# Kernel tuning notes

Measured on AMD Instinct MI355X. Metric: run time of the kernel, lower is better.

Reference implementation:

```python
import jax, jax.numpy as jnp
import numpy as np


def setup_inputs() -> dict:
    key = jax.random.key(0)
    k1, k2 = jax.random.split(key)
    inputs = jax.random.normal(k1, (16, 64, 64, 64), dtype=jnp.float32)  # NCHW, C=embedding_dim
    codebook = jax.random.normal(k2, (1024, 64), dtype=jnp.float32)      # [K, D]
    return {"inputs": inputs, "codebook": codebook}


def reference(inputs, codebook):
    # inputs: [B, C, H, W] -> [B, H, W, C] -> [N, D]
    D = codebook.shape[1]
    x = jnp.transpose(inputs, (0, 2, 3, 1)).reshape(-1, D)  # [N, D]
    distances = (
        jnp.sum(x * x, axis=1, keepdims=True)
        + jnp.sum(codebook * codebook, axis=1)
        - 2.0 * jnp.matmul(x, codebook.T)
    )
    encoding_indices = jnp.argmin(distances, axis=1)[:, None]  # [N, 1]
    return encoding_indices
```

## Files before the change

kernel.cpp:

```cpp
#include <hip/hip_runtime.h>


typedef float f4 __attribute__((ext_vector_type(4)));
typedef float f32x16 __attribute__((ext_vector_type(16)));
typedef short s8v __attribute__((ext_vector_type(8)));
typedef unsigned int u32;

#define D_DIM 64
#define HW    4096
#define ROWSB 128
#define INF_  __builtin_inff()
#define M32(a,b,c) __builtin_amdgcn_mfma_f32_32x32x16_bf16(a,b,c,0,0,0)
#define Z16 (f32x16){0.f,0.f,0.f,0.f,0.f,0.f,0.f,0.f,0.f,0.f,0.f,0.f,0.f,0.f,0.f,0.f}

__device__ __forceinline__ unsigned short bf_rne(float f) {
    u32 u = __builtin_bit_cast(u32, f);
    u32 r = u + 0x7fffu + ((u >> 16) & 1u);
    return (unsigned short)(r >> 16);
}
__device__ __forceinline__ float bf_to_f(unsigned short h) {
    u32 u = ((u32)h) << 16;
    return __builtin_bit_cast(float, u);
}
__device__ __forceinline__ void split3(float f, unsigned short& h,
                                       unsigned short& m, unsigned short& l) {
    h = bf_rne(f);
    float f1 = f - bf_to_f(h);
    m = bf_rne(f1);
    float f2 = f1 - bf_to_f(m);
    l = bf_rne(f2);
}
__device__ __forceinline__ s8v pack8(unsigned short a0, unsigned short a1,
                                     unsigned short a2, unsigned short a3,
                                     unsigned short a4, unsigned short a5,
                                     unsigned short a6, unsigned short a7) {
    uint4 u;
    u.x = a0 | ((u32)a1 << 16);
    u.y = a2 | ((u32)a3 << 16);
    u.z = a4 | ((u32)a5 << 16);
    u.w = a6 | ((u32)a7 << 16);
    return __builtin_bit_cast(s8v, u);
}

__global__ __launch_bounds__(64) void prep_kernel(const float* __restrict__ cb,
                                                  char* __restrict__ wsb) {
    const int blk = blockIdx.x;
    const int lane = threadIdx.x;
    if (blk < 384) {
        const int T = blk / 12;
        const int rem = blk - T * 12;
        const int s = rem / 3;
        const int L = rem - s * 3;
        const int code = T * 32 + (lane & 31);
        const int ch0 = s * 16 + (lane >> 5) * 8;
        const float* src = cb + code * 64 + ch0;
        unsigned short o[8];
#pragma unroll
        for (int j = 0; j < 8; ++j) {
            unsigned short h, m2, l;
            split3(src[j], h, m2, l);
            o[j] = (L == 0) ? h : (L == 1) ? m2 : l;
        }
        uint4 w;
        w.x = o[0] | ((u32)o[1] << 16);
        w.y = o[2] | ((u32)o[3] << 16);
        w.z = o[4] | ((u32)o[5] << 16);
        w.w = o[6] | ((u32)o[7] << 16);
        *(uint4*)(wsb + (size_t)blk * 1024 + lane * 16) = w;
    } else {
        const int k = (blk - 384) * 64 + lane;
        const f4* row = (const f4*)(cb + (size_t)k * 64);
        float sacc = 0.f;
#pragma unroll
        for (int i = 0; i < 16; ++i) {
            f4 v = row[i];
            sacc = fmaf(v.x, v.x, sacc);
            sacc = fmaf(v.y, v.y, sacc);
            sacc = fmaf(v.z, v.z, sacc);
            sacc = fmaf(v.w, v.w, sacc);
        }
        ((float*)(wsb + 384 * 1024))[k] = sacc;
    }
}

__device__ __forceinline__ void gl_lds16(const char* g, char* l) {
    __builtin_amdgcn_global_load_lds(
        (const __attribute__((address_space(1))) void*)g,
        (__attribute__((address_space(3))) void*)l, 16, 0, 0);
}

#define BUILD_A(s) { \
    const float* xr = (const float*)&xs4[w32 + l31][0]; \
    f4 va = *(const f4*)(xr + (s) * 16 + lh8); \
    f4 vb = *(const f4*)(xr + (s) * 16 + lh8 + 4); \
    unsigned short h0,h1,h2,h3,h4,h5,h6,h7; \
    unsigned short q0,q1,q2,q3,q4,q5,q6,q7; \
    unsigned short l0,l1,l2,l3,l4,l5,l6,l7; \
    split3(-2.f * va.x, h0, q0, l0); split3(-2.f * va.y, h1, q1, l1); \
    split3(-2.f * va.z, h2, q2, l2); split3(-2.f * va.w, h3, q3, l3); \
    split3(-2.f * vb.x, h4, q4, l4); split3(-2.f * vb.y, h5, q5, l5); \
    split3(-2.f * vb.z, h6, q6, l6); split3(-2.f * vb.w, h7, q7, l7); \
    Ah##s = pack8(h0,h1,h2,h3,h4,h5,h6,h7); \
    Am##s = pack8(q0,q1,q2,q3,q4,q5,q6,q7); \
    Al##s = pack8(l0,l1,l2,l3,l4,l5,l6,l7); \
}

#define K6(s) \
    c0 = M32(Ah##s, B##s##h, c0); c1 = M32(Ah##s, B##s##m, c1); \
    c0 = M32(Am##s, B##s##h, c0); c1 = M32(Ah##s, B##s##l, c1); \
    c0 = M32(Am##s, B##s##m, c0); c1 = M32(Al##s, B##s##h, c1);

#define UPD(i) { \
    bool pr = (svp[i] < best##i); \
    best##i = pr ? svp[i] : best##i; \
    idx##i  = pr ? kprev : idx##i; \
}
#define UPD_ALL \
    UPD(0)  UPD(1)  UPD(2)  UPD(3)  UPD(4)  UPD(5)  UPD(6)  UPD(7) \
    UPD(8)  UPD(9)  UPD(10) UPD(11) UPD(12) UPD(13) UPD(14) UPD(15)

#define BF1(i, msk) { \
    float ov = __shfl_xor(best##i, msk); \
    int   oi = __shfl_xor(idx##i,  msk); \
    bool pr = (ov < best##i) || (ov == best##i && oi < idx##i); \
    best##i = pr ? ov : best##i; \
    idx##i  = pr ? oi : idx##i; \
}
#define BFALL(msk) \
    BF1(0,msk)  BF1(1,msk)  BF1(2,msk)  BF1(3,msk) \
    BF1(4,msk)  BF1(5,msk)  BF1(6,msk)  BF1(7,msk) \
    BF1(8,msk)  BF1(9,msk)  BF1(10,msk) BF1(11,msk) \
    BF1(12,msk) BF1(13,msk) BF1(14,msk) BF1(15,msk)

__global__ __launch_bounds__(256, 2) void vq_kernel(const float* __restrict__ x,
                                                    const char* __restrict__ wsb,
                                                    int* __restrict__ out) {
    __shared__ __align__(16) char smem[36864];
    __shared__ float sEn[1024];
    f4 (*xs4)[17] = (f4 (*)[17])smem;
    char* const sB = smem;

    const int tid = threadIdx.x;
    const int lane = tid & 63;
    const int w = __builtin_amdgcn_readfirstlane(tid >> 6);
    const int l31 = lane & 31;
    const int lh = lane >> 5;
    const int lh8 = lh * 8;
    const int w32 = w * 32;
    const int wu = w * 3072;
    const int lane16 = lane * 16;
    const int stageoff = wu + lane16;
    const int n0 = blockIdx.x * ROWSB;
    const int b = n0 >> 12;
    const int hw0 = n0 & (HW - 1);

    const float* enp = (const float*)(wsb + 384 * 1024);
#pragma unroll
    for (int q = 0; q < 4; ++q) sEn[q * 256 + tid] = enp[q * 256 + tid];

    {
        const float* g = x + ((size_t)b * D_DIM + w * 16) * HW + hw0 + lane;
        float v[16], v2[16];
#pragma unroll
        for (int i = 0; i < 16; ++i) { v[i] = g[(size_t)i * HW]; v2[i] = g[(size_t)i * HW + 64]; }
#pragma unroll
        for (int j = 0; j < 4; ++j) {
            xs4[lane][w * 4 + j]      = (f4){v[4*j],  v[4*j+1],  v[4*j+2],  v[4*j+3]};
            xs4[lane + 64][w * 4 + j] = (f4){v2[4*j], v2[4*j+1], v2[4*j+2], v2[4*j+3]};
        }
    }
    __syncthreads();

    s8v Ah0, Am0, Al0, Ah1, Am1, Al1, Ah2, Am2, Al2, Ah3, Am3, Al3;
    BUILD_A(0) BUILD_A(1) BUILD_A(2) BUILD_A(3)
    __syncthreads();

    char* b0 = sB;
    char* b1 = sB + 12288;
    char* b2 = sB + 24576;

    gl_lds16(wsb + stageoff,                b0 + wu);
    gl_lds16(wsb + stageoff + 1024,         b0 + wu + 1024);
    gl_lds16(wsb + stageoff + 2048,         b0 + wu + 2048);
    gl_lds16(wsb + 12288 + stageoff,        b1 + wu);
    gl_lds16(wsb + 12288 + stageoff + 1024, b1 + wu + 1024);
    gl_lds16(wsb + 12288 + stageoff + 2048, b1 + wu + 2048);

    float best0=INF_, best1=INF_, best2=INF_, best3=INF_;
    float best4=INF_, best5=INF_, best6=INF_, best7=INF_;
    float best8=INF_, best9=INF_, best10=INF_, best11=INF_;
    float best12=INF_, best13=INF_, best14=INF_, best15=INF_;
    int idx0=0, idx1=0, idx2=0, idx3=0, idx4=0, idx5=0, idx6=0, idx7=0;
    int idx8=0, idx9=0, idx10=0, idx11=0, idx12=0, idx13=0, idx14=0, idx15=0;

    f32x16 svp;
#pragma unroll
    for (int i = 0; i < 16; ++i) svp[i] = INF_;
    int kprev = 0;

    asm volatile("s_waitcnt vmcnt(3)" ::: "memory");
    __builtin_amdgcn_s_barrier();

    const char* gp = wsb + 2 * 12288;
    const char* const gend = wsb + 32 * 12288;
    int p32 = 0;

#pragma unroll 1
    for (int pp = 0; pp < 32; ++pp) {
        gl_lds16(gp + stageoff,        b2 + wu);
        gl_lds16(gp + stageoff + 1024, b2 + wu + 1024);
        gl_lds16(gp + stageoff + 2048, b2 + wu + 2048);

        const char* bb = b0 + lane16;
        s8v B0h = *(const s8v*)(bb +     0), B0m = *(const s8v*)(bb +  1024);
        s8v B0l = *(const s8v*)(bb +  2048);
        s8v B1h = *(const s8v*)(bb +  3072), B1m = *(const s8v*)(bb +  4096);
        s8v B1l = *(const s8v*)(bb +  5120);
        s8v B2h = *(const s8v*)(bb +  6144), B2m = *(const s8v*)(bb +  7168);
        s8v B2l = *(const s8v*)(bb +  8192);
        s8v B3h = *(const s8v*)(bb +  9216), B3m = *(const s8v*)(bb + 10240);
        s8v B3l = *(const s8v*)(bb + 11264);
        const float en0 = sEn[p32 + l31];

        f32x16 c0, c1 = Z16;
#pragma unroll
        for (int i = 0; i < 16; ++i) c0[i] = en0;

        __builtin_amdgcn_s_setprio(1);
        K6(0) K6(1) K6(2) K6(3)
        __builtin_amdgcn_s_setprio(0);

        UPD_ALL

        svp = c0 + c1;
        kprev = p32 + l31;

        asm volatile("s_waitcnt vmcnt(3) lgkmcnt(0)" ::: "memory");
        __builtin_amdgcn_s_barrier();

        { char* t = b0; b0 = b1; b1 = b2; b2 = t; }
        gp += 12288;
        if (gp == gend) gp = wsb;
        p32 += 32;
    }
    asm volatile("s_waitcnt vmcnt(0)" ::: "memory");

    UPD_ALL

    BFALL(1) BFALL(2) BFALL(4) BFALL(8) BFALL(16)

    if (l31 == 0) {
        int* op = out + n0 + w32 + lh * 4;
        int4 q0; q0.x = idx0;  q0.y = idx1;  q0.z = idx2;  q0.w = idx3;
        int4 q1; q1.x = idx4;  q1.y = idx5;  q1.z = idx6;  q1.w = idx7;
        int4 q2; q2.x = idx8;  q2.y = idx9;  q2.z = idx10; q2.w = idx11;
        int4 q3; q3.x = idx12; q3.y = idx13; q3.z = idx14; q3.w = idx15;
        *(int4*)(op)      = q0;
        *(int4*)(op + 8)  = q1;
        *(int4*)(op + 16) = q2;
        *(int4*)(op + 24) = q3;
    }
}

extern "C" void kernel_launch(void* const* d_in, const int* in_sizes, int n_in,
                              void* d_out, int out_size, void* d_ws, size_t ws_size,
                              hipStream_t stream) {
    const float* x  = (const float*)d_in[0];
    const float* cb = (const float*)d_in[1];
    char* wsb = (char*)d_ws;
    int*  out = (int*)d_out;

    prep_kernel<<<dim3(400), dim3(64), 0, stream>>>(cb, wsb);
    vq_kernel<<<dim3(65536 / ROWSB), dim3(256), 0, stream>>>(x, wsb, out);
}
```

Baseline: 112.8 us.

## Software-pipeline codebook LDS reads across sub-steps with ping-pong registers

Splits each 32-code iteration into four sub-steps. Each sub-step issues the LDS loads of B fragments for the next 16-wide K slice into a ping-pong register set while the MFMAs for the current slice run. The running argmin updates are interleaved between these groups, and the next tile's norm initialisation is hoisted. The goal is to hide LDS latency behind MFMA work and lower register pressure from holding all twelve fragments. In exchange it adds many extra workgroup barriers per iteration, which may serialise the waves and cost more than the overlap saves.

```diff
diff --git a/kernel.cpp b/kernel.cpp
--- a/kernel.cpp
+++ b/kernel.cpp
@@ -105,10 +105,17 @@
     Al##s = pack8(l0,l1,l2,l3,l4,l5,l6,l7); \
 }
 
-#define K6(s) \
-    c0 = M32(Ah##s, B##s##h, c0); c1 = M32(Ah##s, B##s##m, c1); \
-    c0 = M32(Am##s, B##s##h, c0); c1 = M32(Ah##s, B##s##l, c1); \
-    c0 = M32(Am##s, B##s##m, c0); c1 = M32(Al##s, B##s##h, c1);
+#define LDB(SET, BASE, SOFF) { \
+    const char* _b = (BASE) + lane16 + (SOFF); \
+    B##SET##h = *(const s8v*)(_b); \
+    B##SET##m = *(const s8v*)(_b + 1024); \
+    B##SET##l = *(const s8v*)(_b + 2048); \
+}
+
+#define K6R(s, SET) \
+    c0 = M32(Ah##s, B##SET##h, c0); c1 = M32(Ah##s, B##SET##m, c1); \
+    c0 = M32(Am##s, B##SET##h, c0); c1 = M32(Ah##s, B##SET##l, c1); \
+    c0 = M32(Am##s, B##SET##m, c0); c1 = M32(Al##s, B##SET##h, c1);
 
 #define UPD(i) { \
     bool pr = (svp[i] < best##i); \
@@ -118,6 +125,11 @@
 #define UPD_ALL \
     UPD(0)  UPD(1)  UPD(2)  UPD(3)  UPD(4)  UPD(5)  UPD(6)  UPD(7) \
     UPD(8)  UPD(9)  UPD(10) UPD(11) UPD(12) UPD(13) UPD(14) UPD(15)
+
+#define FENCE asm volatile("" ::: "memory")
+#define BAR() { FENCE; __builtin_amdgcn_s_barrier(); FENCE; }
+#define SETP1 __builtin_amdgcn_s_setprio(1)
+#define SETP0 __builtin_amdgcn_s_setprio(0)
 
 #define BF1(i, msk) { \
     float ov = __shfl_xor(best##i, msk); \
@@ -198,8 +210,18 @@
     for (int i = 0; i < 16; ++i) svp[i] = INF_;
     int kprev = 0;
 
+    f32x16 c0, c1 = Z16;
+    {
+        const float en0 = sEn[l31];
+#pragma unroll
+        for (int i = 0; i < 16; ++i) c0[i] = en0;
+    }
+
     asm volatile("s_waitcnt vmcnt(3)" ::: "memory");
-    __builtin_amdgcn_s_barrier();
+    BAR();
+
+    s8v BAh, BAm, BAl, BBh, BBm, BBl;
+    LDB(A, b0, 0)
 
     const char* gp = wsb + 2 * 12288;
     const char* const gend = wsb + 32 * 12288;
@@ -210,38 +232,43 @@
         gl_lds16(gp + stageoff,        b2 + wu);
         gl_lds16(gp + stageoff + 1024, b2 + wu + 1024);
         gl_lds16(gp + stageoff + 2048, b2 + wu + 2048);
-
-        const char* bb = b0 + lane16;
-        s8v B0h = *(const s8v*)(bb +     0), B0m = *(const s8v*)(bb +  1024);
-        s8v B0l = *(const s8v*)(bb +  2048);
-        s8v B1h = *(const s8v*)(bb +  3072), B1m = *(const s8v*)(bb +  4096);
-        s8v B1l = *(const s8v*)(bb +  5120);
-        s8v B2h = *(const s8v*)(bb +  6144), B2m = *(const s8v*)(bb +  7168);
-        s8v B2l = *(const s8v*)(bb +  8192);
-        s8v B3h = *(const s8v*)(bb +  9216), B3m = *(const s8v*)(bb + 10240);
-        s8v B3l = *(const s8v*)(bb + 11264);
-        const float en0 = sEn[p32 + l31];
-
-        f32x16 c0, c1 = Z16;
-#pragma unroll
-        for (int i = 0; i < 16; ++i) c0[i] = en0;
-
-        __builtin_amdgcn_s_setprio(1);
-        K6(0) K6(1) K6(2) K6(3)
-        __builtin_amdgcn_s_setprio(0);
-
-        UPD_ALL
-
+        LDB(B, b0, 3072)
+        BAR();
+        asm volatile("s_waitcnt lgkmcnt(0)" ::: "memory");
+        UPD(0) UPD(1) UPD(2) UPD(3)
+        SETP1; K6R(0, A) SETP0;
+        BAR();
+
+        LDB(A, b0, 6144)
+        BAR();
+        asm volatile("s_waitcnt lgkmcnt(0)" ::: "memory");
+        UPD(4) UPD(5) UPD(6) UPD(7)
+        SETP1; K6R(1, B) SETP0;
+        BAR();
+
+        LDB(B, b0, 9216)
+        BAR();
+        asm volatile("s_waitcnt vmcnt(3) lgkmcnt(0)" ::: "memory");
+        UPD(8) UPD(9) UPD(10) UPD(11)
+        SETP1; K6R(2, A) SETP0;
+        BAR();
+
+        LDB(A, b1, 0)
+        const float en_nxt = sEn[((p32 + 32) & 1023) + l31];
+        BAR();
+        asm volatile("s_waitcnt lgkmcnt(0)" ::: "memory");
+        UPD(12) UPD(13) UPD(14) UPD(15)
+        SETP1; K6R(3, B) SETP0;
         svp = c0 + c1;
         kprev = p32 + l31;
-
-        asm volatile("s_waitcnt vmcnt(3) lgkmcnt(0)" ::: "memory");
-        __builtin_amdgcn_s_barrier();
-
+#pragma unroll
+        for (int i = 0; i < 16; ++i) c0[i] = en_nxt;
+        c1 = Z16;
         { char* t = b0; b0 = b1; b1 = b2; b2 = t; }
         gp += 12288;
         if (gp == gend) gp = wsb;
         p32 += 32;
+        BAR();
     }
     asm volatile("s_waitcnt vmcnt(0)" ::: "memory");
 
```

Result: no change. 112.2 us (-0.5%).

## Load codebook B fragments directly from global into registers, double-buffered

Applied to the files above, without the earlier changes.

Replaces the triple-buffered global-to-LDS staging of the split-bf16 codebook tiles, along with its per-iteration barriers, with direct per-lane global loads into two register sets (A/B) that alternate across iterations. The loop is unrolled by two so one tile's loads overlap the other tile's MFMAs, and the energy-bias initialisation moves into a FINISH step. This removes LDS traffic and block-wide synchronisation. In exchange it adds roughly 24 live 128-bit registers, which risks hurting occupancy, and every wave now reads the codebook from L2/global separately.

```diff
diff --git a/kernel.cpp b/kernel.cpp
--- a/kernel.cpp
+++ b/kernel.cpp
@@ -83,12 +83,6 @@
     }
 }
 
-__device__ __forceinline__ void gl_lds16(const char* g, char* l) {
-    __builtin_amdgcn_global_load_lds(
-        (const __attribute__((address_space(1))) void*)g,
-        (__attribute__((address_space(3))) void*)l, 16, 0, 0);
-}
-
 #define BUILD_A(s) { \
     const float* xr = (const float*)&xs4[w32 + l31][0]; \
     f4 va = *(const f4*)(xr + (s) * 16 + lh8); \
@@ -105,10 +99,25 @@
     Al##s = pack8(l0,l1,l2,l3,l4,l5,l6,l7); \
 }
 
-#define K6(s) \
-    c0 = M32(Ah##s, B##s##h, c0); c1 = M32(Ah##s, B##s##m, c1); \
-    c0 = M32(Am##s, B##s##h, c0); c1 = M32(Ah##s, B##s##l, c1); \
-    c0 = M32(Am##s, B##s##m, c0); c1 = M32(Al##s, B##s##h, c1);
+#define LDG(SET, TB) { \
+    const char* _g = (TB) + lane16; \
+    B##SET##0h = *(const s8v*)(_g);          B##SET##0m = *(const s8v*)(_g + 1024); \
+    B##SET##0l = *(const s8v*)(_g + 2048);   B##SET##1h = *(const s8v*)(_g + 3072); \
+    B##SET##1m = *(const s8v*)(_g + 4096);   B##SET##1l = *(const s8v*)(_g + 5120); \
+    B##SET##2h = *(const s8v*)(_g + 6144);   B##SET##2m = *(const s8v*)(_g + 7168); \
+    B##SET##2l = *(const s8v*)(_g + 8192);   B##SET##3h = *(const s8v*)(_g + 9216); \
+    B##SET##3m = *(const s8v*)(_g + 10240);  B##SET##3l = *(const s8v*)(_g + 11264); \
+}
+
+#define K6G(s, SET) \
+    c0 = M32(Ah##s, B##SET##s##h, c0); c1 = M32(Ah##s, B##SET##s##m, c1); \
+    c0 = M32(Am##s, B##SET##s##h, c0); c1 = M32(Ah##s, B##SET##s##l, c1); \
+    c0 = M32(Am##s, B##SET##s##m, c0); c1 = M32(Al##s, B##SET##s##h, c1);
+
+#define K24(SET) \
+    __builtin_amdgcn_s_setprio(1); \
+    K6G(0, SET) K6G(1, SET) K6G(2, SET) K6G(3, SET) \
+    __builtin_amdgcn_s_setprio(0);
 
 #define UPD(i) { \
     bool pr = (svp[i] < best##i); \
@@ -118,6 +127,15 @@
 #define UPD_ALL \
     UPD(0)  UPD(1)  UPD(2)  UPD(3)  UPD(4)  UPD(5)  UPD(6)  UPD(7) \
     UPD(8)  UPD(9)  UPD(10) UPD(11) UPD(12) UPD(13) UPD(14) UPD(15)
+
+#define FINISH(kbase, tn) { \
+    svp = c0 + c1; \
+    kprev = (kbase) + l31; \
+    const float _en = sEn[(((tn) & 31) << 5) + l31]; \
+    _Pragma("unroll") \
+    for (int _i = 0; _i < 16; ++_i) c0[_i] = _en; \
+    c1 = Z16; \
+}
 
 #define BF1(i, msk) { \
     float ov = __shfl_xor(best##i, msk); \
@@ -135,10 +153,8 @@
 __global__ __launch_bounds__(256, 2) void vq_kernel(const float* __restrict__ x,
                                                     const char* __restrict__ wsb,
                                                     int* __restrict__ out) {
-    __shared__ __align__(16) char smem[36864];
+    __shared__ __align__(16) f4 xs4[ROWSB][17];
     __shared__ float sEn[1024];
-    f4 (*xs4)[17] = (f4 (*)[17])smem;
-    char* const sB = smem;
 
     const int tid = threadIdx.x;
     const int lane = tid & 63;
@@ -147,9 +163,7 @@
     const int lh = lane >> 5;
     const int lh8 = lh * 8;
     const int w32 = w * 32;
-    const int wu = w * 3072;
     const int lane16 = lane * 16;
-    const int stageoff = wu + lane16;
     const int n0 = blockIdx.x * ROWSB;
     const int b = n0 >> 12;
     const int hw0 = n0 & (HW - 1);
@@ -173,18 +187,6 @@
 
     s8v Ah0, Am0, Al0, Ah1, Am1, Al1, Ah2, Am2, Al2, Ah3, Am3, Al3;
     BUILD_A(0) BUILD_A(1) BUILD_A(2) BUILD_A(3)
-    __syncthreads();
-
-    char* b0 = sB;
-    char* b1 = sB + 12288;
-    char* b2 = sB + 24576;
-
-    gl_lds16(wsb + stageoff,                b0 + wu);
-    gl_lds16(wsb + stageoff + 1024,         b0 + wu + 1024);
-    gl_lds16(wsb + stageoff + 2048,         b0 + wu + 2048);
-    gl_lds16(wsb + 12288 + stageoff,        b1 + wu);
-    gl_lds16(wsb + 12288 + stageoff + 1024, b1 + wu + 1024);
-    gl_lds16(wsb + 12288 + stageoff + 2048, b1 + wu + 2048);
 
     float best0=INF_, best1=INF_, best2=INF_, best3=INF_;
     float best4=INF_, best5=INF_, best6=INF_, best7=INF_;
@@ -198,52 +200,30 @@
     for (int i = 0; i < 16; ++i) svp[i] = INF_;
     int kprev = 0;
 
-    asm volatile("s_waitcnt vmcnt(3)" ::: "memory");
-    __builtin_amdgcn_s_barrier();
-
-    const char* gp = wsb + 2 * 12288;
-    const char* const gend = wsb + 32 * 12288;
-    int p32 = 0;
+    f32x16 c0, c1 = Z16;
+    {
+        const float en0 = sEn[l31];
+#pragma unroll
+        for (int i = 0; i < 16; ++i) c0[i] = en0;
+    }
+
+    s8v BA0h, BA0m, BA0l, BA1h, BA1m, BA1l, BA2h, BA2m, BA2l, BA3h, BA3m, BA3l;
+    s8v BB0h, BB0m, BB0l, BB1h, BB1m, BB1l, BB2h, BB2m, BB2l, BB3h, BB3m, BB3l;
+
+    LDG(A, wsb)
 
 #pragma unroll 1
-    for (int pp = 0; pp < 32; ++pp) {
-        gl_lds16(gp + stageoff,        b2 + wu);
-        gl_lds16(gp + stageoff + 1024, b2 + wu + 1024);
-        gl_lds16(gp + stageoff + 2048, b2 + wu + 2048);
-
-        const char* bb = b0 + lane16;
-        s8v B0h = *(const s8v*)(bb +     0), B0m = *(const s8v*)(bb +  1024);
-        s8v B0l = *(const s8v*)(bb +  2048);
-        s8v B1h = *(const s8v*)(bb +  3072), B1m = *(const s8v*)(bb +  4096);
-        s8v B1l = *(const s8v*)(bb +  5120);
-        s8v B2h = *(const s8v*)(bb +  6144), B2m = *(const s8v*)(bb +  7168);
-        s8v B2l = *(const s8v*)(bb +  8192);
-        s8v B3h = *(const s8v*)(bb +  9216), B3m = *(const s8v*)(bb + 10240);
-        s8v B3l = *(const s8v*)(bb + 11264);
-        const float en0 = sEn[p32 + l31];
-
-        f32x16 c0, c1 = Z16;
-#pragma unroll
-        for (int i = 0; i < 16; ++i) c0[i] = en0;
-
-        __builtin_amdgcn_s_setprio(1);
-        K6(0) K6(1) K6(2) K6(3)
-        __builtin_amdgcn_s_setprio(0);
-
+    for (int t = 0; t < 16; ++t) {
+        const int tA = 2 * t;
+        LDG(B, wsb + (size_t)(tA + 1) * 12288)
+        K24(A)
+        LDG(A, wsb + (size_t)((tA + 2) & 31) * 12288)
         UPD_ALL
-
-        svp = c0 + c1;
-        kprev = p32 + l31;
-
-        asm volatile("s_waitcnt vmcnt(3) lgkmcnt(0)" ::: "memory");
-        __builtin_amdgcn_s_barrier();
-
-        { char* t = b0; b0 = b1; b1 = b2; b2 = t; }
-        gp += 12288;
-        if (gp == gend) gp = wsb;
-        p32 += 32;
-    }
-    asm volatile("s_waitcnt vmcnt(0)" ::: "memory");
+        FINISH(tA * 32, tA + 1)
+        K24(B)
+        UPD_ALL
+        FINISH((tA + 1) * 32, tA + 2)
+    }
 
     UPD_ALL
 
```

After: 118.0 us. 4.7% more time.
